# Optimization experiments

Measured on AMD Instinct MI355X. Metric: run time of the kernel, lower is better.

## Reference

```python
import jax, jax.numpy as jnp
import numpy as np

T, B, H, W, C = 7, 4, 96, 96, 256
NH, KD = 8, 32  # num_heads, key_dim (attention_filters)


def setup_inputs() -> dict:
    key = jax.random.key(0)
    ks = jax.random.split(key, 8)
    s = 0.02
    return {
        "frames": jax.random.normal(ks[0], (T, B, H, W, C), jnp.float32),
        "t_emb": jax.random.normal(ks[1], (T, C), jnp.float32) * s,  # Embedding(T, C)
        "Wq": jax.random.normal(ks[2], (C, NH, KD), jnp.float32) * s,
        "bq": jnp.zeros((NH, KD), jnp.float32),
        "Wk": jax.random.normal(ks[3], (C, NH, KD), jnp.float32) * s,
        "bk": jnp.zeros((NH, KD), jnp.float32),
        "Wv": jax.random.normal(ks[4], (C, NH, KD), jnp.float32) * s,
        "bv": jnp.zeros((NH, KD), jnp.float32),
        "Wo": jax.random.normal(ks[5], (NH, KD, C), jnp.float32) * s,
        "bo": jnp.zeros((C,), jnp.float32),
    }


def reference(frames, t_emb, Wq, bq, Wk, bk, Wv, bv, Wo, bo):
    # frames: (T, B, H, W, C). Temporal embedding added to keys and queries,
    # values are raw frames. Attention is over the T axis independently at each
    # (b, h, w) location. query_idx defaults to all T frames, so all T single-
    # query MHA calls are batched into one attention with Tq = T.
    emb = t_emb[:, None, None, None, :]            # (T,1,1,1,C)
    kq_in = frames + emb                            # keys and queries share this
    q = jnp.einsum('qbhwc,cnd->qbhwnd', kq_in, Wq) + bq
    k = jnp.einsum('tbhwc,cnd->tbhwnd', kq_in, Wk) + bk
    v = jnp.einsum('tbhwc,cnd->tbhwnd', frames, Wv) + bv
    scale = 1.0 / jnp.sqrt(jnp.asarray(KD, q.dtype))
    scores = jnp.einsum('qbhwnd,tbhwnd->bhwnqt', q, k) * scale  # (B,H,W,NH,Tq,Tk)
    attn = jax.nn.softmax(scores, axis=-1)
    ctx = jnp.einsum('bhwnqt,tbhwnd->qbhwnd', attn, v)
    out = jnp.einsum('qbhwnd,ndc->qbhwc', ctx, Wo) + bo  # (T,B,H,W,C)
    return out
```

## Files before the change

### kernel.cpp

```cpp
#include <hip/hip_runtime.h>
#include <stdint.h>

#define TT 7
#define CC 256
#define NPOSC 36864

typedef unsigned int uint;
typedef unsigned short ushort_t;
typedef __attribute__((ext_vector_type(8))) short short8;
typedef __attribute__((ext_vector_type(4))) float f32x4;

__device__ inline float bf2f(ushort_t u) {
    union { uint i; float f; } v; v.i = ((uint)u) << 16; return v.f;
}
__device__ inline ushort_t f2bf(float f) {
    union { float f; uint i; } v; v.f = f;
    uint i = v.i;
    return (ushort_t)((i + 0x7FFFu + ((i >> 16) & 1u)) >> 16);
}
__device__ inline uint pack2(float a, float b) {
    return (uint)f2bf(a) | (((uint)f2bf(b)) << 16);
}
__device__ inline short8 as_s8(uint4 v) {
    union { uint4 u; short8 s; } x; x.u = v; return x.s;
}

__global__ void prep_kernel(const float* __restrict__ Wq, const float* __restrict__ Wk,
                            const float* __restrict__ Wv, const float* __restrict__ Wo,
                            const float* __restrict__ bq, const float* __restrict__ bk,
                            const float* __restrict__ bv, const float* __restrict__ temb,
                            ushort_t* __restrict__ WTall, ushort_t* __restrict__ WoT,
                            float* __restrict__ biasC)
{
    int bx = blockIdx.x, tid = threadIdx.x;
    if (bx < 64) {
        __shared__ __align__(16) ushort_t tl[64][72];
        int m = bx >> 4, tile = bx & 15;
        int tr = (tile >> 2) * 64, tc = (tile & 3) * 64;
        const float* src = (m == 0) ? Wq : (m == 1) ? Wk : (m == 2) ? Wv : Wo;
        ushort_t* dst = (m < 3) ? (WTall + m * 65536) : WoT;
        int lr = tid >> 2, lc = (tid & 3) * 16;
        const float* sp = src + (size_t)(tr + lr) * 256 + tc + lc;
        #pragma unroll
        for (int q = 0; q < 4; ++q) {
            float4 x = *(const float4*)(sp + q * 4);
            tl[lr][lc + q * 4 + 0] = f2bf(x.x);
            tl[lr][lc + q * 4 + 1] = f2bf(x.y);
            tl[lr][lc + q * 4 + 2] = f2bf(x.z);
            tl[lr][lc + q * 4 + 3] = f2bf(x.w);
        }
        __syncthreads();
        uint w[8];
        #pragma unroll
        for (int j = 0; j < 8; ++j) {
            ushort_t e0 = tl[lc + 2 * j][lr];
            ushort_t e1 = tl[lc + 2 * j + 1][lr];
            w[j] = (uint)e0 | ((uint)e1 << 16);
        }
        uint4 o0, o1;
        o0.x = w[0]; o0.y = w[1]; o0.z = w[2]; o0.w = w[3];
        o1.x = w[4]; o1.y = w[5]; o1.z = w[6]; o1.w = w[7];
        int row = tc + lr;
        int sw = (m < 3) ? ((row & 7) << 3) : 0;
        int c0u = tr + lc;
        *(uint4*)(dst + (size_t)row * 256 + (c0u ^ sw)) = o0;
        *(uint4*)(dst + (size_t)row * 256 + ((c0u + 8) ^ sw)) = o1;
    } else {
        int gid = (bx - 64) * 256 + tid;
        int t = gid / 768, j = gid % 768;
        float val;
        if (j < 256) {
            val = bq[j];
        } else if (j < 512) {
            val = bk[j - 256];
        } else {
            int nd = j - 512;
            float acc = bv[nd];
            for (int c = 0; c < 256; ++c)
                acc -= temb[t * 256 + c] * Wv[(size_t)c * 256 + nd];
            val = acc;
        }
        biasC[t * 768 + j] = val;
    }
}

__launch_bounds__(256, 2)
__global__ void qkv_kernel(const float* __restrict__ frames, const float* __restrict__ temb,
                           const ushort_t* __restrict__ WTsw, const float* __restrict__ biasC,
                           ushort_t* __restrict__ qkvT, int posBase, int Ps)
{
    int t = blockIdx.y;
    int pos0l = blockIdx.x * 128;
    int tid = threadIdx.x;
    int wave = tid >> 6, lane = tid & 63;
    int mh = wave >> 1, nh = wave & 1;
    int l15 = lane & 15, lg = lane >> 4;

    __shared__ __align__(16) ushort_t Atile[2][64][256];

    uint4 Breg[4][8];
    {
        const float* fb = frames + ((size_t)t * NPOSC + posBase + pos0l + nh * 64) * 256;
        #pragma unroll
        for (int kc = 0; kc < 8; ++kc) {
            float4 e0 = *(const float4*)(temb + t * 256 + kc * 32 + lg * 8);
            float4 e1 = *(const float4*)(temb + t * 256 + kc * 32 + lg * 8 + 4);
            #pragma unroll
            for (int nt = 0; nt < 4; ++nt) {
                const float* xp = fb + (size_t)(nt * 16 + l15) * 256 + kc * 32 + lg * 8;
                float4 x0 = *(const float4*)(xp);
                float4 x1 = *(const float4*)(xp + 4);
                uint4 r;
                r.x = pack2(x0.x + e0.x, x0.y + e0.y);
                r.y = pack2(x0.z + e0.z, x0.w + e0.w);
                r.z = pack2(x1.x + e1.x, x1.y + e1.y);
                r.w = pack2(x1.z + e1.z, x1.w + e1.w);
                Breg[nt][kc] = r;
            }
        }
    }

    f32x4 acc[2][4];
    const f32x4 z4 = {0.f, 0.f, 0.f, 0.f};
    #pragma unroll
    for (int mt = 0; mt < 2; ++mt)
        #pragma unroll
        for (int nt = 0; nt < 4; ++nt) acc[mt][nt] = z4;

    const char* wsrc = (const char*)WTsw + (size_t)(wave * 8) * 1024 + (size_t)lane * 16;
    char* lbase = (char*)&Atile[0][0][0] + (size_t)(wave * 8) * 1024;

    #pragma unroll
    for (int i = 0; i < 8; ++i)
        __builtin_amdgcn_global_load_lds(
            (const __attribute__((address_space(1))) void*)(wsrc + i * 1024),
            (__attribute__((address_space(3))) void*)(lbase + i * 1024), 16, 0, 0);
    __syncthreads();

    for (int ndc = 0; ndc < 12; ++ndc) {
        int buf = ndc & 1;
        if (ndc < 11) {
            const char* src = wsrc + (size_t)(ndc + 1) * 32768;
            char* nb = lbase + (size_t)(buf ^ 1) * 32768;
            #pragma unroll
            for (int i = 0; i < 8; ++i)
                __builtin_amdgcn_global_load_lds(
                    (const __attribute__((address_space(1))) void*)(src + i * 1024),
                    (__attribute__((address_space(3))) void*)(nb + i * 1024), 16, 0, 0);
        }
        #pragma unroll
        for (int kc = 0; kc < 8; ++kc) {
            uint4 af[2];
            #pragma unroll
            for (int mt = 0; mt < 2; ++mt) {
                int r = mh * 32 + mt * 16 + l15;
                int colb = (kc * 64 + lg * 16) ^ ((r & 7) << 4);
                af[mt] = *(const uint4*)((const char*)&Atile[buf][r][0] + colb);
            }
            #pragma unroll
            for (int mt = 0; mt < 2; ++mt)
                #pragma unroll
                for (int nt = 0; nt < 4; ++nt)
                    acc[mt][nt] = __builtin_amdgcn_mfma_f32_16x16x32_bf16(
                        as_s8(af[mt]), as_s8(Breg[nt][kc]), acc[mt][nt], 0, 0, 0);
        }
        #pragma unroll
        for (int mt = 0; mt < 2; ++mt) {
            int ndbase = ndc * 64 + mh * 32 + mt * 16 + lg * 4;
            float bi[4];
            #pragma unroll
            for (int i = 0; i < 4; ++i) bi[i] = biasC[t * 768 + ndbase + i];
            #pragma unroll
            for (int nt = 0; nt < 4; ++nt) {
                int posl = pos0l + nh * 64 + nt * 16 + l15;
                #pragma unroll
                for (int i = 0; i < 4; ++i) {
                    float v = acc[mt][nt][i] + bi[i];
                    qkvT[((size_t)(ndbase + i) * 7 + t) * Ps + posl] = f2bf(v);
                }
                acc[mt][nt] = z4;
            }
        }
        __syncthreads();
    }
}

__global__ void attn_kernel(const ushort_t* __restrict__ qkvT, ushort_t* __restrict__ ctxT, int Ps)
{
    int n = blockIdx.y;
    int pos = blockIdx.x * 256 + threadIdx.x;
    const float scale = 0.17677669529663687f;
    float s[7][7];
    #pragma unroll
    for (int a = 0; a < 7; ++a)
        #pragma unroll
        for (int b = 0; b < 7; ++b) s[a][b] = 0.f;

    const ushort_t* qp = qkvT + ((size_t)(n * 32) * 7) * Ps + pos;
    const ushort_t* kp = qkvT + ((size_t)(256 + n * 32) * 7) * Ps + pos;

    for (int d = 0; d < 32; ++d) {
        float qv[7], kv[7];
        #pragma unroll
        for (int i = 0; i < 7; ++i) qv[i] = bf2f(qp[(size_t)(d * 7 + i) * Ps]);
        #pragma unroll
        for (int i = 0; i < 7; ++i) kv[i] = bf2f(kp[(size_t)(d * 7 + i) * Ps]);
        #pragma unroll
        for (int a = 0; a < 7; ++a)
            #pragma unroll
            for (int b = 0; b < 7; ++b) s[a][b] += qv[a] * kv[b];
    }

    #pragma unroll
    for (int a = 0; a < 7; ++a) {
        float mx = -1e30f;
        #pragma unroll
        for (int b = 0; b < 7; ++b) { s[a][b] *= scale; mx = fmaxf(mx, s[a][b]); }
        float sum = 0.f;
        #pragma unroll
        for (int b = 0; b < 7; ++b) {
            float e = exp2f((s[a][b] - mx) * 1.4426950408889634f);
            s[a][b] = e; sum += e;
        }
        float r = 1.0f / sum;
        #pragma unroll
        for (int b = 0; b < 7; ++b) s[a][b] *= r;
    }

    const ushort_t* vp = qkvT + ((size_t)(512 + n * 32) * 7) * Ps + pos;
    const size_t K7P = (size_t)7 * Ps;
    ushort_t* cb = ctxT + (size_t)(n * 32) * K7P + pos;

    #pragma unroll
    for (int dc = 0; dc < 4; ++dc) {
        float o[7][8];
        #pragma unroll
        for (int a = 0; a < 7; ++a)
            #pragma unroll
            for (int j = 0; j < 8; ++j) o[a][j] = 0.f;
        #pragma unroll
        for (int kt = 0; kt < 7; ++kt) {
            float vv[8];
            #pragma unroll
            for (int j = 0; j < 8; ++j)
                vv[j] = bf2f(vp[(size_t)((dc * 8 + j) * 7 + kt) * Ps]);
            #pragma unroll
            for (int a = 0; a < 7; ++a)
                #pragma unroll
                for (int j = 0; j < 8; ++j) o[a][j] += s[a][kt] * vv[j];
        }
        #pragma unroll
        for (int j = 0; j < 8; ++j) {
            ushort_t* cj = cb + (size_t)(dc * 8 + j) * K7P;
            #pragma unroll
            for (int a = 0; a < 7; ++a)
                cj[(size_t)a * Ps] = f2bf(o[a][j]);
        }
    }
}

__launch_bounds__(256, 2)
__global__ void out_kernel(const ushort_t* __restrict__ ctxT, const ushort_t* __restrict__ WoT,
                           const float* __restrict__ bo, float* __restrict__ outp,
                           int posBase, int Ps)
{
    int rows0 = blockIdx.x * 128;
    int c0 = blockIdx.y * 128;
    int tid = threadIdx.x, wave = tid >> 6, lane = tid & 63;
    int mh = wave >> 1, nh = wave & 1;
    int l15 = lane & 15, lg = lane >> 4;
    const size_t K7P = (size_t)7 * Ps;

    __shared__ __align__(16) ushort_t At[2][128][40];
    __shared__ __align__(16) ushort_t Bt[2][128][40];

    int ndl = tid >> 3;
    int rg  = tid & 7;
    int csw = ((((ndl >> 3) ^ (rg & 3)) << 3) | (ndl & 7));

    f32x4 acc[4][4];
    const f32x4 z4 = {0.f, 0.f, 0.f, 0.f};
    #pragma unroll
    for (int mt = 0; mt < 4; ++mt)
        #pragma unroll
        for (int nt = 0; nt < 4; ++nt) acc[mt][nt] = z4;

    {
        const ushort_t* ap = ctxT + (size_t)ndl * K7P + rows0 + rg * 8;
        union { uint4 u; ushort_t s[8]; } ua, ub;
        ua.u = *(const uint4*)ap;
        ub.u = *(const uint4*)(ap + 64);
        #pragma unroll
        for (int i = 0; i < 8; ++i) {
            At[0][rg * 8 + i][csw] = ua.s[i];
            At[0][64 + rg * 8 + i][csw] = ub.s[i];
        }
        #pragma unroll
        for (int p = 0; p < 2; ++p) {
            int ch = p * 256 + tid, row = ch >> 2, q4 = ch & 3;
            uint4 bv_ = *(const uint4*)(WoT + (size_t)(c0 + row) * 256 + q4 * 8);
            *(uint4*)&Bt[0][row][q4 * 8] = bv_;
        }
    }

    #pragma unroll
    for (int kc = 0; kc < 8; ++kc) {
        int buf = kc & 1;
        uint4 na0, na1, nb[2];
        if (kc < 7) {
            const ushort_t* ap = ctxT + (size_t)((kc + 1) * 32 + ndl) * K7P + rows0 + rg * 8;
            na0 = *(const uint4*)ap;
            na1 = *(const uint4*)(ap + 64);
            #pragma unroll
            for (int p = 0; p < 2; ++p) {
                int ch = p * 256 + tid, row = ch >> 2, q4 = ch & 3;
                nb[p] = *(const uint4*)(WoT + (size_t)(c0 + row) * 256 + (kc + 1) * 32 + q4 * 8);
            }
        }
        __syncthreads();
        if (kc < 7) {
            union { uint4 u; ushort_t s[8]; } ua, ub;
            ua.u = na0; ub.u = na1;
            #pragma unroll
            for (int i = 0; i < 8; ++i) {
                At[buf ^ 1][rg * 8 + i][csw] = ua.s[i];
                At[buf ^ 1][64 + rg * 8 + i][csw] = ub.s[i];
            }
            #pragma unroll
            for (int p = 0; p < 2; ++p) {
                int ch = p * 256 + tid, row = ch >> 2, q4 = ch & 3;
                *(uint4*)&Bt[buf ^ 1][row][q4 * 8] = nb[p];
            }
        }
        uint4 af[4], bfr[4];
        #pragma unroll
        for (int mt = 0; mt < 4; ++mt) {
            int r = mh * 64 + mt * 16 + l15;
            af[mt] = *(const uint4*)&At[buf][r][(lg ^ ((r >> 3) & 3)) << 3];
        }
        #pragma unroll
        for (int nt = 0; nt < 4; ++nt)
            bfr[nt] = *(const uint4*)&Bt[buf][nh * 64 + nt * 16 + l15][lg * 8];
        #pragma unroll
        for (int mt = 0; mt < 4; ++mt)
            #pragma unroll
            for (int nt = 0; nt < 4; ++nt)
                acc[mt][nt] = __builtin_amdgcn_mfma_f32_16x16x32_bf16(
                    as_s8(af[mt]), as_s8(bfr[nt]), acc[mt][nt], 0, 0, 0);
    }

    int t = rows0 / Ps;
    int prow = rows0 - t * Ps;
    size_t obase = (size_t)t * NPOSC + posBase + prow;
    #pragma unroll
    for (int nt = 0; nt < 4; ++nt) {
        int col = c0 + nh * 64 + nt * 16 + l15;
        float bov = bo[col];
        #pragma unroll
        for (int mt = 0; mt < 4; ++mt) {
            #pragma unroll
            for (int i = 0; i < 4; ++i) {
                int r = mh * 64 + mt * 16 + lg * 4 + i;
                outp[(obase + r) * 256 + col] = acc[mt][nt][i] + bov;
            }
        }
    }
}

extern "C" void kernel_launch(void* const* d_in, const int* in_sizes, int n_in,
                              void* d_out, int out_size, void* d_ws, size_t ws_size,
                              hipStream_t stream)
{
    const float* frames = (const float*)d_in[0];
    const float* temb   = (const float*)d_in[1];
    const float* Wq = (const float*)d_in[2];
    const float* bq = (const float*)d_in[3];
    const float* Wk = (const float*)d_in[4];
    const float* bk = (const float*)d_in[5];
    const float* Wv = (const float*)d_in[6];
    const float* bv = (const float*)d_in[7];
    const float* Wo = (const float*)d_in[8];
    const float* bo = (const float*)d_in[9];
    float* outp = (float*)d_out;

    char* w = (char*)d_ws;
    ushort_t* WTall = (ushort_t*)w;
    ushort_t* WoT   = (ushort_t*)(w + 393216);
    float*    biasC = (float*)(w + 524288);
    const size_t fixed = 557056;

    int s = 1;
    for (; s < 16; s *= 2) {
        size_t Ps_ = (size_t)NPOSC / s;
        size_t need = fixed + 768ull * 7 * Ps_ * 2 + 7ull * Ps_ * 256 * 2;
        if (need <= ws_size) break;
    }
    int Ps = NPOSC / s;
    ushort_t* qkvT = (ushort_t*)(w + fixed);
    ushort_t* ctxp = (ushort_t*)(w + fixed + (size_t)768 * 7 * Ps * 2);

    prep_kernel<<<85, 256, 0, stream>>>(Wq, Wk, Wv, Wo, bq, bk, bv, temb,
                                        WTall, WoT, biasC);
    for (int sl = 0; sl < s; ++sl) {
        int posBase = sl * Ps;
        qkv_kernel<<<dim3(Ps / 128, 7), 256, 0, stream>>>(frames, temb, WTall, biasC,
                                                          qkvT, posBase, Ps);
        attn_kernel<<<dim3(Ps / 256, 8), 256, 0, stream>>>(qkvT, ctxp, Ps);
        out_kernel<<<dim3(7 * Ps / 128, 2), 256, 0, stream>>>(ctxp, WoT, bo, outp,
                                                              posBase, Ps);
    }
}
```

Baseline: 858.2 us.

## Shrink QKV tiles, stage outputs through LDS for coalesced stores, raise occupancy

The QKV GEMM kernel now gives each wave 32 positions and walks 32-wide output chunks (24 iterations instead of 12). This halves the register-held B fragments and the LDS weight tiles so three blocks can fit per CU. Results are transposed through a per-wave LDS tile and written as 16-byte vector stores instead of scattered 2-byte stores, and the conversions use the hardware packed bf16 convert instruction. The attention kernel processes value dims in chunks of 4 with a non-unrolled loop and a launch bound of 4 blocks, to cut register pressure. The trade-off is more loop iterations and barriers, plus extra LDS traffic.

```diff
diff --git a/kernel.cpp b/kernel.cpp
--- a/kernel.cpp
+++ b/kernel.cpp
@@ -20,6 +20,11 @@
 }
 __device__ inline uint pack2(float a, float b) {
     return (uint)f2bf(a) | (((uint)f2bf(b)) << 16);
+}
+__device__ inline uint cvtpk(float lo, float hi) {
+    uint r;
+    asm("v_cvt_pk_bf16_f32 %0, %1, %2" : "=v"(r) : "v"(lo), "v"(hi));
+    return r;
 }
 __device__ inline short8 as_s8(uint4 v) {
     union { uint4 u; short8 s; } x; x.u = v; return x.s;
@@ -84,7 +89,7 @@
     }
 }
 
-__launch_bounds__(256, 2)
+__launch_bounds__(256, 3)
 __global__ void qkv_kernel(const float* __restrict__ frames, const float* __restrict__ temb,
                            const ushort_t* __restrict__ WTsw, const float* __restrict__ biasC,
                            ushort_t* __restrict__ qkvT, int posBase, int Ps)
@@ -93,57 +98,57 @@
     int pos0l = blockIdx.x * 128;
     int tid = threadIdx.x;
     int wave = tid >> 6, lane = tid & 63;
-    int mh = wave >> 1, nh = wave & 1;
     int l15 = lane & 15, lg = lane >> 4;
 
-    __shared__ __align__(16) ushort_t Atile[2][64][256];
-
-    uint4 Breg[4][8];
+    __shared__ __align__(16) ushort_t Atile[2][32][256];
+    __shared__ __align__(16) ushort_t Ttile[4][32][40];
+
+    uint4 Breg[2][8];
     {
-        const float* fb = frames + ((size_t)t * NPOSC + posBase + pos0l + nh * 64) * 256;
+        const float* fb = frames + ((size_t)t * NPOSC + posBase + pos0l + wave * 32) * 256;
         #pragma unroll
         for (int kc = 0; kc < 8; ++kc) {
             float4 e0 = *(const float4*)(temb + t * 256 + kc * 32 + lg * 8);
             float4 e1 = *(const float4*)(temb + t * 256 + kc * 32 + lg * 8 + 4);
             #pragma unroll
-            for (int nt = 0; nt < 4; ++nt) {
+            for (int nt = 0; nt < 2; ++nt) {
                 const float* xp = fb + (size_t)(nt * 16 + l15) * 256 + kc * 32 + lg * 8;
                 float4 x0 = *(const float4*)(xp);
                 float4 x1 = *(const float4*)(xp + 4);
                 uint4 r;
-                r.x = pack2(x0.x + e0.x, x0.y + e0.y);
-                r.y = pack2(x0.z + e0.z, x0.w + e0.w);
-                r.z = pack2(x1.x + e1.x, x1.y + e1.y);
-                r.w = pack2(x1.z + e1.z, x1.w + e1.w);
+                r.x = cvtpk(x0.x + e0.x, x0.y + e0.y);
+                r.y = cvtpk(x0.z + e0.z, x0.w + e0.w);
+                r.z = cvtpk(x1.x + e1.x, x1.y + e1.y);
+                r.w = cvtpk(x1.z + e1.z, x1.w + e1.w);
                 Breg[nt][kc] = r;
             }
         }
     }
 
-    f32x4 acc[2][4];
+    f32x4 acc[2][2];
     const f32x4 z4 = {0.f, 0.f, 0.f, 0.f};
     #pragma unroll
     for (int mt = 0; mt < 2; ++mt)
         #pragma unroll
-        for (int nt = 0; nt < 4; ++nt) acc[mt][nt] = z4;
-
-    const char* wsrc = (const char*)WTsw + (size_t)(wave * 8) * 1024 + (size_t)lane * 16;
-    char* lbase = (char*)&Atile[0][0][0] + (size_t)(wave * 8) * 1024;
-
-    #pragma unroll
-    for (int i = 0; i < 8; ++i)
+        for (int nt = 0; nt < 2; ++nt) acc[mt][nt] = z4;
+
+    const char* wsrc = (const char*)WTsw + (size_t)(wave * 4) * 1024 + (size_t)lane * 16;
+    char* lbase = (char*)&Atile[0][0][0] + (size_t)(wave * 4) * 1024;
+
+    #pragma unroll
+    for (int i = 0; i < 4; ++i)
         __builtin_amdgcn_global_load_lds(
             (const __attribute__((address_space(1))) void*)(wsrc + i * 1024),
             (__attribute__((address_space(3))) void*)(lbase + i * 1024), 16, 0, 0);
     __syncthreads();
 
-    for (int ndc = 0; ndc < 12; ++ndc) {
+    for (int ndc = 0; ndc < 24; ++ndc) {
         int buf = ndc & 1;
-        if (ndc < 11) {
-            const char* src = wsrc + (size_t)(ndc + 1) * 32768;
-            char* nb = lbase + (size_t)(buf ^ 1) * 32768;
-            #pragma unroll
-            for (int i = 0; i < 8; ++i)
+        if (ndc < 23) {
+            const char* src = wsrc + (size_t)(ndc + 1) * 16384;
+            char* nb = lbase + (size_t)(buf ^ 1) * 16384;
+            #pragma unroll
+            for (int i = 0; i < 4; ++i)
                 __builtin_amdgcn_global_load_lds(
                     (const __attribute__((address_space(1))) void*)(src + i * 1024),
                     (__attribute__((address_space(3))) void*)(nb + i * 1024), 16, 0, 0);
@@ -153,38 +158,50 @@
             uint4 af[2];
             #pragma unroll
             for (int mt = 0; mt < 2; ++mt) {
-                int r = mh * 32 + mt * 16 + l15;
+                int r = mt * 16 + l15;
                 int colb = (kc * 64 + lg * 16) ^ ((r & 7) << 4);
                 af[mt] = *(const uint4*)((const char*)&Atile[buf][r][0] + colb);
             }
             #pragma unroll
             for (int mt = 0; mt < 2; ++mt)
                 #pragma unroll
-                for (int nt = 0; nt < 4; ++nt)
+                for (int nt = 0; nt < 2; ++nt)
                     acc[mt][nt] = __builtin_amdgcn_mfma_f32_16x16x32_bf16(
                         as_s8(af[mt]), as_s8(Breg[nt][kc]), acc[mt][nt], 0, 0, 0);
         }
         #pragma unroll
         for (int mt = 0; mt < 2; ++mt) {
-            int ndbase = ndc * 64 + mh * 32 + mt * 16 + lg * 4;
-            float bi[4];
-            #pragma unroll
-            for (int i = 0; i < 4; ++i) bi[i] = biasC[t * 768 + ndbase + i];
-            #pragma unroll
-            for (int nt = 0; nt < 4; ++nt) {
-                int posl = pos0l + nh * 64 + nt * 16 + l15;
-                #pragma unroll
-                for (int i = 0; i < 4; ++i) {
-                    float v = acc[mt][nt][i] + bi[i];
-                    qkvT[((size_t)(ndbase + i) * 7 + t) * Ps + posl] = f2bf(v);
-                }
+            int ndbase = ndc * 32 + mt * 16 + lg * 4;
+            float b0 = biasC[t * 768 + ndbase + 0];
+            float b1 = biasC[t * 768 + ndbase + 1];
+            float b2 = biasC[t * 768 + ndbase + 2];
+            float b3 = biasC[t * 768 + ndbase + 3];
+            #pragma unroll
+            for (int nt = 0; nt < 2; ++nt) {
+                int pl = nt * 16 + l15;
+                uint p0 = cvtpk(acc[mt][nt][0] + b0, acc[mt][nt][1] + b1);
+                uint p1 = cvtpk(acc[mt][nt][2] + b2, acc[mt][nt][3] + b3);
+                int nl = mt * 16 + lg * 4;
+                Ttile[wave][nl + 0][pl] = (ushort_t)p0;
+                Ttile[wave][nl + 1][pl] = (ushort_t)(p0 >> 16);
+                Ttile[wave][nl + 2][pl] = (ushort_t)p1;
+                Ttile[wave][nl + 3][pl] = (ushort_t)(p1 >> 16);
                 acc[mt][nt] = z4;
             }
         }
+        #pragma unroll
+        for (int r = 0; r < 2; ++r) {
+            int ndr = r * 16 + (lane >> 2);
+            int seg = lane & 3;
+            uint4 v = *(const uint4*)&Ttile[wave][ndr][seg * 8];
+            int nd = ndc * 32 + ndr;
+            *(uint4*)(qkvT + ((size_t)nd * 7 + t) * Ps + pos0l + wave * 32 + seg * 8) = v;
+        }
         __syncthreads();
     }
 }
 
+__launch_bounds__(256, 4)
 __global__ void attn_kernel(const ushort_t* __restrict__ qkvT, ushort_t* __restrict__ ctxT, int Ps)
 {
     int n = blockIdx.y;
@@ -231,27 +248,27 @@
     const size_t K7P = (size_t)7 * Ps;
     ushort_t* cb = ctxT + (size_t)(n * 32) * K7P + pos;
 
-    #pragma unroll
-    for (int dc = 0; dc < 4; ++dc) {
-        float o[7][8];
+    #pragma unroll 1
+    for (int dc = 0; dc < 8; ++dc) {
+        float o[7][4];
         #pragma unroll
         for (int a = 0; a < 7; ++a)
             #pragma unroll
-            for (int j = 0; j < 8; ++j) o[a][j] = 0.f;
+            for (int j = 0; j < 4; ++j) o[a][j] = 0.f;
         #pragma unroll
         for (int kt = 0; kt < 7; ++kt) {
-            float vv[8];
-            #pragma unroll
-            for (int j = 0; j < 8; ++j)
-                vv[j] = bf2f(vp[(size_t)((dc * 8 + j) * 7 + kt) * Ps]);
+            float vv[4];
+            #pragma unroll
+            for (int j = 0; j < 4; ++j)
+                vv[j] = bf2f(vp[(size_t)((dc * 4 + j) * 7 + kt) * Ps]);
             #pragma unroll
             for (int a = 0; a < 7; ++a)
                 #pragma unroll
-                for (int j = 0; j < 8; ++j) o[a][j] += s[a][kt] * vv[j];
-        }
-        #pragma unroll
-        for (int j = 0; j < 8; ++j) {
-            ushort_t* cj = cb + (size_t)(dc * 8 + j) * K7P;
+                for (int j = 0; j < 4; ++j) o[a][j] += s[a][kt] * vv[j];
+        }
+        #pragma unroll
+        for (int j = 0; j < 4; ++j) {
+            ushort_t* cj = cb + (size_t)(dc * 4 + j) * K7P;
             #pragma unroll
             for (int a = 0; a < 7; ++a)
                 cj[(size_t)a * Ps] = f2bf(o[a][j]);
```

Result: faster. 786.7 us (-8.3%).
